# Optimization experiments

Measured on AMD Instinct MI355X. Metric: run time of the kernel, lower is better.

## Reference

```python
import jax, jax.numpy as jnp
import numpy as np

NUM_HEADS = 16
HEAD_SIZE = 64
CTXT_LEN = 2048
N_EMBED = 1024
BATCH = 2


def setup_inputs() -> dict:
    key = jax.random.key(0)
    ks = jax.random.split(key, 5)
    s = 0.02  # realistic init scale for weights
    return {
        "x": jax.random.normal(ks[0], (BATCH, CTXT_LEN, N_EMBED), dtype=jnp.float32),
        "Wk": jax.random.normal(ks[1], (N_EMBED, NUM_HEADS * HEAD_SIZE), dtype=jnp.float32) * s,
        "bk": jnp.zeros((NUM_HEADS * HEAD_SIZE,), dtype=jnp.float32),
        "Wq": jax.random.normal(ks[2], (N_EMBED, NUM_HEADS * HEAD_SIZE), dtype=jnp.float32) * s,
        "bq": jnp.zeros((NUM_HEADS * HEAD_SIZE,), dtype=jnp.float32),
        "Wv": jax.random.normal(ks[3], (N_EMBED, NUM_HEADS * HEAD_SIZE), dtype=jnp.float32) * s,
        "bv": jnp.zeros((NUM_HEADS * HEAD_SIZE,), dtype=jnp.float32),
        "Wo": jax.random.normal(ks[4], (NUM_HEADS * HEAD_SIZE, N_EMBED), dtype=jnp.float32) * s,
        "bo": jnp.zeros((N_EMBED,), dtype=jnp.float32),
    }


def reference(x, Wk, bk, Wq, bq, Wv, bv, Wo, bo):
    B, T, E = x.shape
    H, D = NUM_HEADS, HEAD_SIZE
    # QKV projections -> [B, T, H, D]
    k = (x @ Wk + bk).reshape(B, T, H, D)
    q = (x @ Wq + bq).reshape(B, T, H, D)
    v = (x @ Wv + bv).reshape(B, T, H, D)
    # NOTE: source scales by 1/sqrt(n_embed), not 1/sqrt(head_size)
    scale = 1.0 / (E ** 0.5)
    wei = jnp.einsum('bthd,bshd->bhts', q, k) * scale  # [B, H, T, T]
    causal = jnp.tril(jnp.ones((T, T), dtype=bool))
    wei = jnp.where(causal, wei, -jnp.inf)
    wei = jax.nn.softmax(wei, axis=-1)
    # dropout p=0.0 -> identity
    out = jnp.einsum('bhts,bshd->bthd', wei, v).reshape(B, T, H * D)
    return out @ Wo + bo
```

## Files before the change

kernel.cpp:

```cpp
#include <hip/hip_runtime.h>

#define NH 16
#define HS 64
#define T_CTX 2048
#define NE 1024
#define NB 2
#define BT (NB*T_CTX)
#define HD (NH*HS)

typedef unsigned short u16;
typedef __bf16 bf16_t;
typedef bf16_t bf16x8 __attribute__((ext_vector_type(8)));
typedef float f32x4 __attribute__((ext_vector_type(4)));
typedef u16 u16x8 __attribute__((ext_vector_type(8)));
typedef u16 u16x4 __attribute__((ext_vector_type(4)));

#define GLDS(gp, lp) __builtin_amdgcn_global_load_lds( \
    (const __attribute__((address_space(1))) void*)(gp), \
    (__attribute__((address_space(3))) void*)(lp), 16, 0, 0)

__device__ __forceinline__ u16 f2bf(float f) {
  union { float f; unsigned u; } x; x.f = f;
  return (u16)((x.u + 0x7fffu + ((x.u >> 16) & 1u)) >> 16);
}
__device__ __forceinline__ float bf2f(u16 u) {
  union { unsigned u; float f; } x; x.u = ((unsigned)u) << 16;
  return x.f;
}
__device__ __forceinline__ unsigned pack_bf2(float hi, float lo) {
  union { float f; unsigned u; } H, L; H.f = hi; L.f = lo;
  return __builtin_amdgcn_perm(H.u + 0x8000u, L.u + 0x8000u, 0x07060302);
}

__global__ __launch_bounds__(256) void k_prep_x(const float* __restrict__ x,
                                                u16* __restrict__ xb) {
  int i = blockIdx.x * blockDim.x + threadIdx.x;
  float4 v = ((const float4*)x)[i];
  ushort4 o;
  o.x = f2bf(v.x); o.y = f2bf(v.y); o.z = f2bf(v.z); o.w = f2bf(v.w);
  ((ushort4*)xb)[i] = o;
}

__global__ __launch_bounds__(256) void k_prep_w(
    const float* __restrict__ W0, const float* __restrict__ W1,
    const float* __restrict__ W2, const float* __restrict__ W3,
    u16* __restrict__ T0, u16* __restrict__ T1,
    u16* __restrict__ T2, u16* __restrict__ T3) {
  const float* W; u16* T;
  switch (blockIdx.z) {
    case 0: W = W0; T = T0; break;
    case 1: W = W1; T = T1; break;
    case 2: W = W2; T = T2; break;
    default: W = W3; T = T3; break;
  }
  __shared__ u16 tile[64 * 72];
  int k0 = blockIdx.x * 64, n0 = blockIdx.y * 64;
  int tid = threadIdx.x;
#pragma unroll
  for (int it = 0; it < 4; ++it) {
    int ci = tid + it * 256;
    int k = ci >> 4, c = ci & 15;
    float4 v = *(const float4*)&W[(size_t)(k0 + k) * NE + n0 + c * 4];
    int n = c * 4;
    tile[(n + 0) * 72 + k] = f2bf(v.x);
    tile[(n + 1) * 72 + k] = f2bf(v.y);
    tile[(n + 2) * 72 + k] = f2bf(v.z);
    tile[(n + 3) * 72 + k] = f2bf(v.w);
  }
  __syncthreads();
#pragma unroll
  for (int it = 0; it < 2; ++it) {
    int co = tid + it * 256;
    int n = co >> 3, c = co & 7;
    u16x8 v = *(const u16x8*)&tile[n * 72 + c * 8];
    *(u16x8*)&T[(size_t)(n0 + n) * NE + k0 + c * 8] = v;
  }
}

__device__ __forceinline__ void gemm_core(
    const u16* __restrict__ A, const u16* __restrict__ Bt,
    int m0, int n0, u16* As, u16* Bs, f32x4 (&acc)[4][4]) {
  const int tid = threadIdx.x, lane = tid & 63, w = tid >> 6;
  const int wm = (w >> 1) * 64, wn = (w & 1) * 64;
  const int q = lane >> 4, l16 = lane & 15;
#pragma unroll
  for (int i = 0; i < 4; ++i)
#pragma unroll
    for (int j = 0; j < 4; ++j)
#pragma unroll
      for (int r = 0; r < 4; ++r) acc[i][j][r] = 0.f;

  for (int k0 = 0; k0 < NE; k0 += 32) {
#pragma unroll
    for (int s2 = 0; s2 < 2; ++s2) {
      int ci = w * 64 + lane + s2 * 256;
      int row = ci >> 2, cc = ci & 3;
      GLDS(A  + (size_t)(m0 + row) * NE + k0 + cc * 8, As + (size_t)(w * 64 + s2 * 256) * 8);
      GLDS(Bt + (size_t)(n0 + row) * NE + k0 + cc * 8, Bs + (size_t)(w * 64 + s2 * 256) * 8);
    }
    __syncthreads();
    bf16x8 av[4], bv4[4];
#pragma unroll
    for (int i = 0; i < 4; ++i) av[i]  = *(const bf16x8*)&As[(wm + i * 16 + l16) * 32 + q * 8];
#pragma unroll
    for (int j = 0; j < 4; ++j) bv4[j] = *(const bf16x8*)&Bs[(wn + j * 16 + l16) * 32 + q * 8];
#pragma unroll
    for (int i = 0; i < 4; ++i)
#pragma unroll
      for (int j = 0; j < 4; ++j)
        acc[i][j] = __builtin_amdgcn_mfma_f32_16x16x32_bf16(av[i], bv4[j], acc[i][j], 0, 0, 0);
    __syncthreads();
  }
}

__global__ __launch_bounds__(256) void k_gemm_qkv(
    const u16* __restrict__ xb, const u16* __restrict__ Wt,
    const float* __restrict__ bq, const float* __restrict__ bk,
    const float* __restrict__ bv, u16* __restrict__ Qw,
    u16* __restrict__ Kw, u16* __restrict__ Vtw) {
  __shared__ u16 As[128 * 32], Bs[128 * 32];
  __shared__ u16 Es[128 * 132];
  const int z = blockIdx.z;
  const u16* W = Wt + (size_t)z * NE * HD;
  const float* bias = (z == 0) ? bq : (z == 1 ? bk : bv);
  const float scale = (z == 0) ? 0.03125f * 1.4426950408889634f : 1.0f;
  const int m0 = blockIdx.y * 128, n0 = blockIdx.x * 128;
  f32x4 acc[4][4];
  gemm_core(xb, W, m0, n0, As, Bs, acc);
  const int tid = threadIdx.x;
  const int lane = tid & 63, w = tid >> 6;
  const int wm = (w >> 1) * 64, wn = (w & 1) * 64, q = lane >> 4, l16 = lane & 15;
  const int bb = m0 >> 11;
  if (z == 2) {
#pragma unroll
    for (int j = 0; j < 4; ++j) {
      int n = wn + j * 16 + l16;
      float bn = bias[n0 + n];
#pragma unroll
      for (int i = 0; i < 4; ++i) {
        int m = wm + i * 16 + q * 4;
        u16x4 pk;
#pragma unroll
        for (int r = 0; r < 4; ++r) pk[r] = f2bf(acc[i][j][r] + bn);
        *(u16x4*)&Es[n * 132 + m] = pk;
      }
    }
    __syncthreads();
#pragma unroll
    for (int it = 0; it < 8; ++it) {
      int idx = it * 256 + tid;
      int dl = idx >> 4, c = idx & 15;
      u16x8 v = *(const u16x8*)&Es[dl * 132 + c * 8];
      int ng = n0 + dl, h = ng >> 6, d = ng & 63;
      int tt = (m0 & (T_CTX - 1)) + c * 8;
      *(u16x8*)&Vtw[((size_t)((bb * NH + h) * HS + d)) * T_CTX + tt] = v;
    }
  } else {
    u16* dst = (z == 0) ? Qw : Kw;
#pragma unroll
    for (int j = 0; j < 4; ++j) {
      int n = wn + j * 16 + l16;
      float bn = bias[n0 + n];
#pragma unroll
      for (int i = 0; i < 4; ++i)
#pragma unroll
        for (int r = 0; r < 4; ++r) {
          int m = wm + i * 16 + q * 4 + r;
          Es[m * 132 + n] = f2bf((acc[i][j][r] + bn) * scale);
        }
    }
    __syncthreads();
#pragma unroll
    for (int it = 0; it < 8; ++it) {
      int idx = it * 256 + tid;
      int tl = idx >> 4, c = idx & 15;
      u16x8 v = *(const u16x8*)&Es[tl * 132 + c * 8];
      int ng = n0 + c * 8, h = ng >> 6, d = ng & 63;
      int tt = (m0 & (T_CTX - 1)) + tl;
      *(u16x8*)&dst[(((size_t)(bb * NH + h)) * T_CTX + tt) * HS + d] = v;
    }
  }
}

__device__ __forceinline__ void stage_kv(const u16* __restrict__ Kp,
                                         const u16* __restrict__ Vp,
                                         int k0, u16* KsB, u16* VsB, int tid) {
#pragma unroll
  for (int it = 0; it < 2; ++it) {
    int ci = tid + it * 256;
    int row = ci >> 3, cc = ci & 7;
    int sw = (cc ^ (row & 7)) * 8;
    GLDS(Kp + (size_t)(k0 + row) * HS + sw, KsB + ci * 8);
    GLDS(Vp + (size_t)row * T_CTX + k0 + sw, VsB + ci * 8);
  }
}

__global__ __launch_bounds__(256) void k_attn(
    const u16* __restrict__ Qw, const u16* __restrict__ Kw,
    const u16* __restrict__ Vtw, u16* __restrict__ op0,
    u16* __restrict__ op1, u16* __restrict__ op2,
    float* __restrict__ lsum) {
  __shared__ u16 Ks[2 * 64 * 64];
  __shared__ u16 Vs[2 * 64 * 64];
  __shared__ u16 Ps[128 * 64];

  const int bh = blockIdx.y;
  const int x = blockIdx.x;
  const int qt = 15 - x / 3;
  const int part = x - (15 - qt) * 3;
  const int ntiles = 2 * (qt + 1);
  const int npt = (ntiles + 2) / 3;
  const int klo = part * npt;
  const int khi = min(klo + npt, ntiles);
  const int qbase = qt * 128;

  const u16* Qp = Qw + (size_t)bh * T_CTX * HS;
  const u16* Kp = Kw + (size_t)bh * T_CTX * HS;
  const u16* Vp = Vtw + (size_t)bh * HS * T_CTX;

  const int tid = threadIdx.x, lane = tid & 63, w = tid >> 6;
  const int q = lane >> 4, c = lane & 15;
  const int rbase = w * 32;

  bf16x8 aq[2][2];
#pragma unroll
  for (int i = 0; i < 2; ++i)
#pragma unroll
    for (int s = 0; s < 2; ++s)
      aq[i][s] = *(const bf16x8*)&Qp[(size_t)(qbase + rbase + i * 16 + c) * HS + s * 32 + q * 8];

  f32x4 o[2][4];
  float lrow[2] = {0.f, 0.f};
#pragma unroll
  for (int i = 0; i < 2; ++i)
#pragma unroll
    for (int j = 0; j < 4; ++j)
#pragma unroll
      for (int r = 0; r < 4; ++r) o[i][j][r] = 0.f;

  if (klo < khi) stage_kv(Kp, Vp, klo * 64, Ks, Vs, tid);

  for (int kt = klo; kt < khi; ++kt) {
    const int k0 = kt * 64;
    const int buf = (kt - klo) & 1;
    u16* KsB = Ks + buf * 4096;
    u16* VsB = Vs + buf * 4096;
    __syncthreads();
    if (kt + 1 < khi)
      stage_kv(Kp, Vp, k0 + 64, Ks + (buf ^ 1) * 4096, Vs + (buf ^ 1) * 4096, tid);

    f32x4 s[4][2];
#pragma unroll
    for (int i2 = 0; i2 < 4; ++i2) {
      int krow = i2 * 16 + c;
      bf16x8 kf0 = *(const bf16x8*)&KsB[krow * 64 + ((0 + q) ^ (krow & 7)) * 8];
      bf16x8 kf1 = *(const bf16x8*)&KsB[krow * 64 + ((4 + q) ^ (krow & 7)) * 8];
#pragma unroll
      for (int j2 = 0; j2 < 2; ++j2) {
        f32x4 z4 = {0.f, 0.f, 0.f, 0.f};
        z4 = __builtin_amdgcn_mfma_f32_16x16x32_bf16(kf0, aq[j2][0], z4, 0, 0, 0);
        s[i2][j2] = __builtin_amdgcn_mfma_f32_16x16x32_bf16(kf1, aq[j2][1], z4, 0, 0, 0);
      }
    }

    if (k0 + 63 > qbase + rbase) {
#pragma unroll
      for (int i2 = 0; i2 < 4; ++i2)
#pragma unroll
        for (int j2 = 0; j2 < 2; ++j2)
#pragma unroll
          for (int r = 0; r < 4; ++r) {
            int key = k0 + i2 * 16 + q * 4 + r;
            int qrow = qbase + rbase + j2 * 16 + c;
            if (key > qrow) s[i2][j2][r] = -1e30f;
          }
    }

#pragma unroll
    for (int j2 = 0; j2 < 2; ++j2) {
      const int qrow = rbase + j2 * 16 + c;
#pragma unroll
      for (int i2 = 0; i2 < 4; ++i2) {
        float p[4];
#pragma unroll
        for (int r = 0; r < 4; ++r) {
          p[r] = __builtin_amdgcn_exp2f(fminf(s[i2][j2][r], 120.f));
          lrow[j2] += p[r];
        }
        uint2 pd;
        pd.x = pack_bf2(p[1], p[0]);
        pd.y = pack_bf2(p[3], p[2]);
        *(uint2*)&Ps[qrow * 64 + ((i2 * 2 + (q >> 1)) ^ (c & 7)) * 8 + (q & 1) * 4] = pd;
      }
    }

#pragma unroll
    for (int ks = 0; ks < 2; ++ks) {
      bf16x8 bv4[4];
#pragma unroll
      for (int j = 0; j < 4; ++j) {
        int d = j * 16 + c;
        bv4[j] = *(const bf16x8*)&VsB[d * 64 + ((ks * 4 + q) ^ (d & 7)) * 8];
      }
#pragma unroll
      for (int i = 0; i < 2; ++i) {
        int qrow = rbase + i * 16 + c;
        bf16x8 a = *(const bf16x8*)&Ps[qrow * 64 + ((ks * 4 + q) ^ (c & 7)) * 8];
#pragma unroll
        for (int j = 0; j < 4; ++j)
          o[i][j] = __builtin_amdgcn_mfma_f32_16x16x32_bf16(a, bv4[j], o[i][j], 0, 0, 0);
      }
    }
  }

  u16* op = (part == 0) ? op0 : (part == 1 ? op1 : op2);
  const size_t row0 = (size_t)bh * T_CTX + qbase;
#pragma unroll
  for (int i = 0; i < 2; ++i) {
    lrow[i] += __shfl_xor(lrow[i], 16, 64);
    lrow[i] += __shfl_xor(lrow[i], 32, 64);
  }
  if (q == 0) {
#pragma unroll
    for (int i = 0; i < 2; ++i)
      lsum[(size_t)part * 65536 + row0 + rbase + i * 16 + c] = lrow[i];
  }
#pragma unroll
  for (int i = 0; i < 2; ++i)
#pragma unroll
    for (int r = 0; r < 4; ++r) {
      size_t t = row0 + rbase + i * 16 + q * 4 + r;
#pragma unroll
      for (int j = 0; j < 4; ++j)
        op[t * 64 + j * 16 + c] = f2bf(o[i][j][r]);
    }
}

__global__ __launch_bounds__(256) void k_combine(
    const u16* __restrict__ op0, const u16* __restrict__ op1,
    const u16* __restrict__ op2, const float* __restrict__ lsum,
    u16* __restrict__ att) {
  int idx = blockIdx.x * 256 + threadIdx.x;
  int row = idx >> 3, oct = idx & 7;
  float l0 = lsum[row], l1 = lsum[65536 + row], l2 = lsum[131072 + row];
  float inv = 1.f / (l0 + l1 + l2);
  u16x8 a = *(const u16x8*)&op0[(size_t)row * 64 + oct * 8];
  u16x8 b = *(const u16x8*)&op1[(size_t)row * 64 + oct * 8];
  u16x8 d = *(const u16x8*)&op2[(size_t)row * 64 + oct * 8];
  u16x8 ov;
#pragma unroll
  for (int e = 0; e < 8; ++e)
    ov[e] = f2bf((bf2f(a[e]) + bf2f(b[e]) + bf2f(d[e])) * inv);
  int bh = row >> 11, t = row & 2047, bb = bh >> 4, h = bh & 15;
  *(u16x8*)&att[((size_t)(bb * T_CTX + t)) * HD + h * 64 + oct * 8] = ov;
}

__global__ __launch_bounds__(256) void k_gemm_out(
    const u16* __restrict__ attb, const u16* __restrict__ Wot,
    const float* __restrict__ bo, float* __restrict__ out) {
  __shared__ u16 As[128 * 32], Bs[128 * 32];
  const int m0 = blockIdx.y * 128, n0 = blockIdx.x * 128;
  f32x4 acc[4][4];
  gemm_core(attb, Wot, m0, n0, As, Bs, acc);
  const int lane = threadIdx.x & 63, w = threadIdx.x >> 6;
  const int wm = (w >> 1) * 64, wn = (w & 1) * 64, q = lane >> 4, l16 = lane & 15;
#pragma unroll
  for (int j = 0; j < 4; ++j) {
    int n = n0 + wn + j * 16 + l16;
    float bn = bo[n];
#pragma unroll
    for (int i = 0; i < 4; ++i)
#pragma unroll
      for (int r = 0; r < 4; ++r) {
        int m = m0 + wm + i * 16 + q * 4 + r;
        out[(size_t)m * NE + n] = acc[i][j][r] + bn;
      }
  }
}

extern "C" void kernel_launch(void* const* d_in, const int* in_sizes, int n_in,
                              void* d_out, int out_size, void* d_ws, size_t ws_size,
                              hipStream_t stream) {
  (void)in_sizes; (void)n_in; (void)out_size; (void)ws_size;
  const float* x  = (const float*)d_in[0];
  const float* Wk = (const float*)d_in[1];
  const float* bk = (const float*)d_in[2];
  const float* Wq = (const float*)d_in[3];
  const float* bq = (const float*)d_in[4];
  const float* Wv = (const float*)d_in[5];
  const float* bv = (const float*)d_in[6];
  const float* Wo = (const float*)d_in[7];
  const float* bo = (const float*)d_in[8];
  float* out = (float*)d_out;

  u16* base = (u16*)d_ws;
  const size_t M = 1024 * 1024;
  u16* xb   = base;
  u16* Wt   = base + 4 * M;
  u16* Wot  = base + 7 * M;
  u16* Qw   = base + 8 * M;
  u16* Kw   = base + 12 * M;
  u16* Vtw  = base + 16 * M;
  u16* op0  = base + 20 * M;
  u16* op1  = base + 24 * M;
  u16* op2  = base;
  float* lsum = (float*)(base + 4 * M);
  u16* attw = base + 12 * M;

  k_prep_x<<<dim3(BT * NE / 4 / 256), 256, 0, stream>>>(x, xb);
  k_prep_w<<<dim3(16, 16, 4), 256, 0, stream>>>(
      Wq, Wk, Wv, Wo, Wt, Wt + (size_t)NE * HD, Wt + (size_t)2 * NE * HD, Wot);
  k_gemm_qkv<<<dim3(8, 32, 3), 256, 0, stream>>>(xb, Wt, bq, bk, bv, Qw, Kw, Vtw);
  k_attn<<<dim3(48, 32), 256, 0, stream>>>(Qw, Kw, Vtw, op0, op1, op2, lsum);
  k_combine<<<dim3(2048), 256, 0, stream>>>(op0, op1, op2, lsum, attw);
  k_gemm_out<<<dim3(8, 32), 256, 0, stream>>>(attw, Wot, bo, out);
}
```

Measured before the change: 222.0 us.

## Keep softmax probabilities in registers and retile output projection GEMM

The attention kernel permutes K rows on load so the QK^T MFMA output layout matches the PV MFMA A-operand layout. That lets probabilities be packed straight from registers instead of round-tripping through a shared-memory P buffer, and the causal mask key index is remapped to match. The freed shared memory plus a launch-bounds occupancy hint of 5 aim for more resident blocks. Separately, the output GEMM moves to 64x128 tiles with twice as many blocks, using its own non-pipelined loop, to improve CU fill at the cost of more B-tile reloads.

```diff
diff --git a/kernel.cpp b/kernel.cpp
--- a/kernel.cpp
+++ b/kernel.cpp
@@ -189,20 +189,20 @@
   for (int it = 0; it < 2; ++it) {
     int ci = tid + it * 256;
     int row = ci >> 3, cc = ci & 7;
+    int prow = (row & 32) | ((row & 12) << 1) | ((row & 16) >> 2) | (row & 3);
     int sw = (cc ^ (row & 7)) * 8;
-    GLDS(Kp + (size_t)(k0 + row) * HS + sw, KsB + ci * 8);
+    GLDS(Kp + (size_t)(k0 + prow) * HS + sw, KsB + ci * 8);
     GLDS(Vp + (size_t)row * T_CTX + k0 + sw, VsB + ci * 8);
   }
 }
 
-__global__ __launch_bounds__(256) void k_attn(
+__global__ __launch_bounds__(256, 5) void k_attn(
     const u16* __restrict__ Qw, const u16* __restrict__ Kw,
     const u16* __restrict__ Vtw, u16* __restrict__ op0,
     u16* __restrict__ op1, u16* __restrict__ op2,
     float* __restrict__ lsum) {
   __shared__ u16 Ks[2 * 64 * 64];
   __shared__ u16 Vs[2 * 64 * 64];
-  __shared__ u16 Ps[128 * 64];
 
   const int bh = blockIdx.y;
   const int x = blockIdx.x;
@@ -270,29 +270,22 @@
         for (int j2 = 0; j2 < 2; ++j2)
 #pragma unroll
           for (int r = 0; r < 4; ++r) {
-            int key = k0 + i2 * 16 + q * 4 + r;
+            int key = k0 + ((i2 >> 1) << 5) + (q << 3) + ((i2 & 1) << 2) + r;
             int qrow = qbase + rbase + j2 * 16 + c;
             if (key > qrow) s[i2][j2][r] = -1e30f;
           }
     }
 
 #pragma unroll
-    for (int j2 = 0; j2 < 2; ++j2) {
-      const int qrow = rbase + j2 * 16 + c;
-#pragma unroll
-      for (int i2 = 0; i2 < 4; ++i2) {
-        float p[4];
+    for (int i2 = 0; i2 < 4; ++i2)
+#pragma unroll
+      for (int j2 = 0; j2 < 2; ++j2)
 #pragma unroll
         for (int r = 0; r < 4; ++r) {
-          p[r] = __builtin_amdgcn_exp2f(fminf(s[i2][j2][r], 120.f));
-          lrow[j2] += p[r];
+          float p = __builtin_amdgcn_exp2f(fminf(s[i2][j2][r], 120.f));
+          s[i2][j2][r] = p;
+          lrow[j2] += p;
         }
-        uint2 pd;
-        pd.x = pack_bf2(p[1], p[0]);
-        pd.y = pack_bf2(p[3], p[2]);
-        *(uint2*)&Ps[qrow * 64 + ((i2 * 2 + (q >> 1)) ^ (c & 7)) * 8 + (q & 1) * 4] = pd;
-      }
-    }
 
 #pragma unroll
     for (int ks = 0; ks < 2; ++ks) {
@@ -304,11 +297,14 @@
       }
 #pragma unroll
       for (int i = 0; i < 2; ++i) {
-        int qrow = rbase + i * 16 + c;
-        bf16x8 a = *(const bf16x8*)&Ps[qrow * 64 + ((ks * 4 + q) ^ (c & 7)) * 8];
+        union { uint4 u; bf16x8 b; } af;
+        af.u.x = pack_bf2(s[2 * ks][i][1],     s[2 * ks][i][0]);
+        af.u.y = pack_bf2(s[2 * ks][i][3],     s[2 * ks][i][2]);
+        af.u.z = pack_bf2(s[2 * ks + 1][i][1], s[2 * ks + 1][i][0]);
+        af.u.w = pack_bf2(s[2 * ks + 1][i][3], s[2 * ks + 1][i][2]);
 #pragma unroll
         for (int j = 0; j < 4; ++j)
-          o[i][j] = __builtin_amdgcn_mfma_f32_16x16x32_bf16(a, bv4[j], o[i][j], 0, 0, 0);
+          o[i][j] = __builtin_amdgcn_mfma_f32_16x16x32_bf16(af.b, bv4[j], o[i][j], 0, 0, 0);
       }
     }
   }
@@ -358,18 +354,49 @@
 __global__ __launch_bounds__(256) void k_gemm_out(
     const u16* __restrict__ attb, const u16* __restrict__ Wot,
     const float* __restrict__ bo, float* __restrict__ out) {
-  __shared__ u16 As[128 * 32], Bs[128 * 32];
-  const int m0 = blockIdx.y * 128, n0 = blockIdx.x * 128;
-  f32x4 acc[4][4];
-  gemm_core(attb, Wot, m0, n0, As, Bs, acc);
-  const int lane = threadIdx.x & 63, w = threadIdx.x >> 6;
-  const int wm = (w >> 1) * 64, wn = (w & 1) * 64, q = lane >> 4, l16 = lane & 15;
+  __shared__ u16 As[64 * 32], Bs[128 * 32];
+  const int m0 = blockIdx.y * 64, n0 = blockIdx.x * 128;
+  const int tid = threadIdx.x, lane = tid & 63, w = tid >> 6;
+  const int wm = (w & 1) * 32, wn = (w >> 1) * 64;
+  const int q = lane >> 4, l16 = lane & 15;
+  f32x4 acc[2][4];
+#pragma unroll
+  for (int i = 0; i < 2; ++i)
+#pragma unroll
+    for (int j = 0; j < 4; ++j)
+#pragma unroll
+      for (int r = 0; r < 4; ++r) acc[i][j][r] = 0.f;
+
+  for (int k0 = 0; k0 < NE; k0 += 32) {
+    {
+      int row = tid >> 2, cc = tid & 3;
+      GLDS(attb + (size_t)(m0 + row) * NE + k0 + cc * 8, As + (size_t)tid * 8);
+    }
+#pragma unroll
+    for (int s2 = 0; s2 < 2; ++s2) {
+      int ci = tid + s2 * 256;
+      int row = ci >> 2, cc = ci & 3;
+      GLDS(Wot + (size_t)(n0 + row) * NE + k0 + cc * 8, Bs + (size_t)ci * 8);
+    }
+    __syncthreads();
+    bf16x8 av[2], bv4[4];
+#pragma unroll
+    for (int i = 0; i < 2; ++i) av[i]  = *(const bf16x8*)&As[(wm + i * 16 + l16) * 32 + q * 8];
+#pragma unroll
+    for (int j = 0; j < 4; ++j) bv4[j] = *(const bf16x8*)&Bs[(wn + j * 16 + l16) * 32 + q * 8];
+#pragma unroll
+    for (int i = 0; i < 2; ++i)
+#pragma unroll
+      for (int j = 0; j < 4; ++j)
+        acc[i][j] = __builtin_amdgcn_mfma_f32_16x16x32_bf16(av[i], bv4[j], acc[i][j], 0, 0, 0);
+    __syncthreads();
+  }
 #pragma unroll
   for (int j = 0; j < 4; ++j) {
     int n = n0 + wn + j * 16 + l16;
     float bn = bo[n];
 #pragma unroll
-    for (int i = 0; i < 4; ++i)
+    for (int i = 0; i < 2; ++i)
 #pragma unroll
       for (int r = 0; r < 4; ++r) {
         int m = m0 + wm + i * 16 + q * 4 + r;
@@ -413,5 +440,5 @@
   k_gemm_qkv<<<dim3(8, 32, 3), 256, 0, stream>>>(xb, Wt, bq, bk, bv, Qw, Kw, Vtw);
   k_attn<<<dim3(48, 32), 256, 0, stream>>>(Qw, Kw, Vtw, op0, op1, op2, lsum);
   k_combine<<<dim3(2048), 256, 0, stream>>>(op0, op1, op2, lsum, attw);
-  k_gemm_out<<<dim3(8, 32), 256, 0, stream>>>(attw, Wot, bo, out);
-}
+  k_gemm_out<<<dim3(8, 64), 256, 0, stream>>>(attw, Wot, bo, out);
+}
```

Result: slower. 296.3 us (+33.5%).
